# Optimization experiments

Hardware: AMD Instinct MI355X
Metric: run time of the kernel (lower is better)

## Reference

```python
import jax, jax.numpy as jnp
import numpy as np

TAU = 0.5

def setup_inputs() -> dict:
    key = jax.random.key(0)
    ks = jax.random.split(key, 8)
    B_Nq, B_Ns, C, H, W = 16, 16, 512, 32, 32
    f_q = jax.random.normal(ks[0], (B_Nq, C, H, W), dtype=jnp.float32)
    f_s = jax.random.normal(ks[1], (B_Ns, C, H, W), dtype=jnp.float32)
    # depthwise 1x1 convs with groups=dim, bias=False -> per-channel scalar weights [C]
    w_cca_q = jax.random.normal(ks[2], (C,), dtype=jnp.float32)
    w_cca_k = jax.random.normal(ks[3], (C,), dtype=jnp.float32)
    w_cca_v = jax.random.normal(ks[4], (C,), dtype=jnp.float32)
    w_sca_q = jax.random.normal(ks[5], (C,), dtype=jnp.float32)
    w_sca_k = jax.random.normal(ks[6], (C,), dtype=jnp.float32)
    lam = jnp.float32(0.1)
    return {"f_q": f_q, "f_s": f_s, "w_cca_q": w_cca_q, "w_cca_k": w_cca_k,
            "w_cca_v": w_cca_v, "w_sca_q": w_sca_q, "w_sca_k": w_sca_k, "lam": lam}

def _dw(x, w):
    # depthwise 1x1 conv, no bias == per-channel scale; x: [B,C,H,W], w: [C]
    return x * w[None, :, None, None]

def reference(f_q, f_s, w_cca_q, w_cca_k, w_cca_v, w_sca_q, w_sca_k, lam):
    B_Nq, C, H, W = f_q.shape
    B_Ns = f_s.shape[0]
    P = H * W
    qc = _dw(f_q, w_cca_q).reshape(B_Nq, C, P)          # [B,C,P]
    kc_mean = _dw(f_s, w_cca_k).reshape(B_Ns, C, P).mean(axis=0)  # [C,P]
    vc_mean = _dw(f_s, w_cca_v).reshape(B_Ns, C, P).mean(axis=0)  # [C,P]
    # channel attention: [B,C,C]
    Ac = jax.nn.softmax(jnp.einsum('bcp,dp->bcd', qc, kc_mean) / P, axis=-1)
    f_cca_q = jnp.einsum('bcd,dp->bcp', Ac, vc_mean).reshape(B_Nq, C, H, W)
    qs = _dw(f_cca_q, w_sca_q).reshape(B_Nq, C, P)      # [B,C,P]
    ks_mean = _dw(f_s, w_sca_k).reshape(B_Ns, C, P).mean(axis=0)  # [C,P]
    # spatial affinity: [B,P,P]
    M = jnp.einsum('bcp,cq->bpq', qs, ks_mean) / (TAU * C)
    alpha = jax.nn.softmax(M.mean(axis=-1), axis=-1)    # [B_Nq,P]
    beta = jax.nn.softmax(M.mean(axis=-2), axis=-1)     # [B_Nq,P]
    beta_mean = jnp.broadcast_to(beta.mean(axis=0, keepdims=True), (B_Ns, P))
    Fq_out = f_q + lam * f_cca_q
    return (Fq_out, alpha, beta_mean)
```

## Files before the change

### kernel.cpp

```cpp
#include <hip/hip_runtime.h>

typedef __bf16 bf16;
typedef __bf16 bf16x4 __attribute__((ext_vector_type(4)));
typedef __bf16 bf16x8 __attribute__((ext_vector_type(8)));
typedef float f32x4 __attribute__((ext_vector_type(4)));


#define GLL16(g, l)                                                             \
    __builtin_amdgcn_global_load_lds((const __attribute__((address_space(1))) void*)(g), \
                                     (__attribute__((address_space(3))) void*)(l), 16, 0, 0)

__device__ inline float wave_reduce_sum(float v) {
#pragma unroll
    for (int m = 32; m >= 1; m >>= 1) v += __shfl_xor(v, m, 64);
    return v;
}
__device__ inline float wave_reduce_max(float v) {
#pragma unroll
    for (int m = 32; m >= 1; m >>= 1) v = fmaxf(v, __shfl_xor(v, m, 64));
    return v;
}

__global__ void k_prep(const float* __restrict__ fs, const float* __restrict__ fq,
                       float* __restrict__ fsm32, bf16* __restrict__ fsm16,
                       bf16* __restrict__ fsmT, bf16* __restrict__ fq16) {
    __shared__ bf16 tile[32][33];
    int bx = blockIdx.x, by = blockIdx.y;
    int p0 = bx * 32, c0 = by * 32;
    int t = threadIdx.x, tx = t & 31, ty = t >> 5;
#pragma unroll
    for (int i = 0; i < 4; ++i) {
        size_t off = (size_t)(c0 + ty + 8 * i) * 1024 + p0 + tx;
        float s = 0.f;
#pragma unroll
        for (int b = 0; b < 16; ++b) s += fs[(size_t)b * 524288 + off];
        s *= (1.f / 16.f);
        fsm32[off] = s;
        bf16 h = (bf16)s;
        fsm16[off] = h;
        tile[ty + 8 * i][tx] = h;
    }
    __syncthreads();
#pragma unroll
    for (int i = 0; i < 4; ++i)
        fsmT[(size_t)(p0 + ty + 8 * i) * 512 + c0 + tx] = tile[tx][ty + 8 * i];
    int blk = by * 32 + bx;
    const float4* f4 = (const float4*)fq;
#pragma unroll
    for (int i = 0; i < 16; ++i) {
        int idx = blk * 4096 + i * 256 + t;
        float4 v = f4[idx];
        bf16x4 h4 = {(bf16)v.x, (bf16)v.y, (bf16)v.z, (bf16)v.w};
        *(bf16x4*)(fq16 + (size_t)idx * 4) = h4;
    }
}

__global__ void k_u(const float* __restrict__ fsm32, const float* __restrict__ wsq,
                    const float* __restrict__ wsk, float* __restrict__ u,
                    float* __restrict__ rm) {
    int c = blockIdx.x;
    int t = threadIdx.x;
    float s = 0.f;
#pragma unroll
    for (int j = 0; j < 4; ++j) s += fsm32[(size_t)c * 1024 + t + 256 * j];
    s = wave_reduce_sum(s);
    __shared__ float red[4];
    int w = t >> 6, lane = t & 63;
    if (lane == 0) red[w] = s;
    __syncthreads();
    if (t == 0) {
        float rmv = (red[0] + red[1] + red[2] + red[3]) * (1.f / 1024.f);
        rm[c] = rmv;
        u[c] = wsq[c] * wsk[c] * rmv * (1.f / 256.f);
    }
}

__global__ void k_gemm1(const bf16* __restrict__ A, const bf16* __restrict__ B,
                        float* __restrict__ G) {
    __shared__ alignas(16) bf16 As[64 * 32];
    __shared__ alignas(16) bf16 Bs[128 * 32];
    const int dt = blockIdx.x, ct = blockIdx.y, b = blockIdx.z;
    const int t = threadIdx.x, w = t >> 6, lane = t & 63;
    const int quad = lane >> 4, r15 = lane & 15;
    const int wr = w & 1, wc = w >> 1;
    const bf16* Abase = A + ((size_t)(b * 512 + ct * 64)) * 1024;
    const bf16* Bbase = B + ((size_t)(dt * 128)) * 1024;
    const int pr = t >> 2;
    const int gc = (t & 3) ^ ((pr >> 1) & 3);
    f32x4 acc[2][4] = {};
    for (int k0 = 0; k0 < 1024; k0 += 32) {
        GLL16(Abase + (size_t)pr * 1024 + k0 + gc * 8, As + t * 8);
        GLL16(Bbase + (size_t)pr * 1024 + k0 + gc * 8, Bs + t * 8);
        GLL16(Bbase + (size_t)(pr + 64) * 1024 + k0 + gc * 8, Bs + (t + 256) * 8);
        __syncthreads();
        bf16x8 af[2], bfr[4];
#pragma unroll
        for (int mi = 0; mi < 2; ++mi) {
            int R = wr * 32 + mi * 16 + r15;
            int sc = quad ^ ((R >> 1) & 3);
            af[mi] = *(const bf16x8*)(As + R * 32 + sc * 8);
        }
#pragma unroll
        for (int j = 0; j < 4; ++j) {
            int R = wc * 64 + j * 16 + r15;
            int sc = quad ^ ((R >> 1) & 3);
            bfr[j] = *(const bf16x8*)(Bs + R * 32 + sc * 8);
        }
#pragma unroll
        for (int mi = 0; mi < 2; ++mi)
#pragma unroll
            for (int j = 0; j < 4; ++j)
                acc[mi][j] = __builtin_amdgcn_mfma_f32_16x16x32_bf16(af[mi], bfr[j], acc[mi][j], 0, 0, 0);
        __syncthreads();
    }
#pragma unroll
    for (int mi = 0; mi < 2; ++mi) {
        float* g = G + ((size_t)(b * 512 + ct * 64 + wr * 32 + mi * 16 + quad * 4)) * 512 +
                   dt * 128 + wc * 64 + r15;
#pragma unroll
        for (int j = 0; j < 4; ++j)
#pragma unroll
            for (int ii = 0; ii < 4; ++ii)
                g[(size_t)ii * 512 + j * 16] = acc[mi][j][ii];
    }
}

__global__ void k_softmax_ac(const float* __restrict__ G, const float* __restrict__ wq,
                             const float* __restrict__ wk, const float* __restrict__ wv,
                             const float* __restrict__ rm, bf16* __restrict__ Acw,
                             float* __restrict__ r) {
    int row = blockIdx.x * 4 + (threadIdx.x >> 6);
    int lane = threadIdx.x & 63;
    int c = row & 511;
    const float* g = G + (size_t)row * 512;
    float sc = wq[c] * (1.f / 1024.f);
    float v[8];
    float mx = -3.4e38f;
#pragma unroll
    for (int j = 0; j < 8; ++j) {
        int d = lane + 64 * j;
        v[j] = g[d] * sc * wk[d];
        mx = fmaxf(mx, v[j]);
    }
    mx = wave_reduce_max(mx);
    float sum = 0.f;
#pragma unroll
    for (int j = 0; j < 8; ++j) {
        v[j] = __expf(v[j] - mx);
        sum += v[j];
    }
    sum = wave_reduce_sum(sum);
    float inv = 1.f / sum;
    bf16* o = Acw + (size_t)row * 512;
    float rsum = 0.f;
#pragma unroll
    for (int j = 0; j < 8; ++j) {
        int d = lane + 64 * j;
        float aw = v[j] * inv * wv[d];
        o[d] = (bf16)aw;
        rsum += aw * rm[d];
    }
    rsum = wave_reduce_sum(rsum);
    if (lane == 0) r[row] = rsum;
}

__global__ void k_t(const bf16* __restrict__ Acw, const float* __restrict__ u,
                    float* __restrict__ tbp) {
    int half = blockIdx.z, b = blockIdx.y;
    int d = blockIdx.x * 256 + threadIdx.x;
    const bf16* base = Acw + (size_t)b * 262144 + (size_t)half * 256 * 512 + d;
    const float* uu = u + half * 256;
    float s0 = 0.f, s1 = 0.f, s2 = 0.f, s3 = 0.f;
#pragma unroll 4
    for (int c = 0; c < 256; c += 4) {
        s0 += uu[c] * (float)base[(size_t)c * 512];
        s1 += uu[c + 1] * (float)base[(size_t)(c + 1) * 512];
        s2 += uu[c + 2] * (float)base[(size_t)(c + 2) * 512];
        s3 += uu[c + 3] * (float)base[(size_t)(c + 3) * 512];
    }
    tbp[(half * 16 + b) * 512 + d] = (s0 + s1) + (s2 + s3);
}

__global__ void k_gemm2(const bf16* __restrict__ A, const bf16* __restrict__ B,
                        const float* __restrict__ fq, const float* __restrict__ lamp,
                        float* __restrict__ out) {
    __shared__ alignas(16) bf16 As[64 * 32];
    __shared__ alignas(16) bf16 Bs[128 * 32];
    const int pt = blockIdx.x, ct = blockIdx.y, b = blockIdx.z;
    const int t = threadIdx.x, w = t >> 6, lane = t & 63;
    const int quad = lane >> 4, r15 = lane & 15;
    const int wr = w & 1, wc = w >> 1;
    const bf16* Abase = A + ((size_t)(b * 512 + ct * 64)) * 512;
    const bf16* Bbase = B + ((size_t)(pt * 128)) * 512;
    const int pr = t >> 2;
    const int gc = (t & 3) ^ ((pr >> 1) & 3);
    f32x4 acc[2][4] = {};
    for (int k0 = 0; k0 < 512; k0 += 32) {
        GLL16(Abase + (size_t)pr * 512 + k0 + gc * 8, As + t * 8);
        GLL16(Bbase + (size_t)pr * 512 + k0 + gc * 8, Bs + t * 8);
        GLL16(Bbase + (size_t)(pr + 64) * 512 + k0 + gc * 8, Bs + (t + 256) * 8);
        __syncthreads();
        bf16x8 af[2], bfr[4];
#pragma unroll
        for (int mi = 0; mi < 2; ++mi) {
            int R = wr * 32 + mi * 16 + r15;
            int sc = quad ^ ((R >> 1) & 3);
            af[mi] = *(const bf16x8*)(As + R * 32 + sc * 8);
        }
#pragma unroll
        for (int j = 0; j < 4; ++j) {
            int R = wc * 64 + j * 16 + r15;
            int sc = quad ^ ((R >> 1) & 3);
            bfr[j] = *(const bf16x8*)(Bs + R * 32 + sc * 8);
        }
#pragma unroll
        for (int mi = 0; mi < 2; ++mi)
#pragma unroll
            for (int j = 0; j < 4; ++j)
                acc[mi][j] = __builtin_amdgcn_mfma_f32_16x16x32_bf16(af[mi], bfr[j], acc[mi][j], 0, 0, 0);
        __syncthreads();
    }
    float lam = lamp[0];
#pragma unroll
    for (int mi = 0; mi < 2; ++mi) {
        size_t rowbase = (size_t)(b * 512 + ct * 64 + wr * 32 + mi * 16 + quad * 4);
#pragma unroll
        for (int j = 0; j < 4; ++j)
#pragma unroll
            for (int ii = 0; ii < 4; ++ii) {
                size_t idx = (rowbase + ii) * 1024 + pt * 128 + wc * 64 + j * 16 + r15;
                out[idx] = fq[idx] + lam * acc[mi][j][ii];
            }
    }
}

__global__ void k_logits(const float* __restrict__ tbp, const float* __restrict__ r,
                         const float* __restrict__ wsq, const float* __restrict__ wsk,
                         const float* __restrict__ fsm32, float* __restrict__ alog,
                         float* __restrict__ blog) {
    int z = blockIdx.y, pq = blockIdx.x * 256 + threadIdx.x;
    if (z < 16) {
        const float* t0 = tbp + z * 512;
        const float* t1 = tbp + (16 + z) * 512;
        float s0 = 0.f, s1 = 0.f, s2 = 0.f, s3 = 0.f;
#pragma unroll 2
        for (int d = 0; d < 512; d += 4) {
            s0 += (t0[d] + t1[d]) * fsm32[(size_t)d * 1024 + pq];
            s1 += (t0[d + 1] + t1[d + 1]) * fsm32[(size_t)(d + 1) * 1024 + pq];
            s2 += (t0[d + 2] + t1[d + 2]) * fsm32[(size_t)(d + 2) * 1024 + pq];
            s3 += (t0[d + 3] + t1[d + 3]) * fsm32[(size_t)(d + 3) * 1024 + pq];
        }
        alog[z * 1024 + pq] = (s0 + s1) + (s2 + s3);
    } else {
        int b = z - 16;
        const float* rb = r + b * 512;
        float s0 = 0.f, s1 = 0.f, s2 = 0.f, s3 = 0.f;
#pragma unroll 2
        for (int c = 0; c < 512; c += 4) {
            s0 += rb[c] * wsq[c] * wsk[c] * (1.f / 256.f) * fsm32[(size_t)c * 1024 + pq];
            s1 += rb[c + 1] * wsq[c + 1] * wsk[c + 1] * (1.f / 256.f) * fsm32[(size_t)(c + 1) * 1024 + pq];
            s2 += rb[c + 2] * wsq[c + 2] * wsk[c + 2] * (1.f / 256.f) * fsm32[(size_t)(c + 2) * 1024 + pq];
            s3 += rb[c + 3] * wsq[c + 3] * wsk[c + 3] * (1.f / 256.f) * fsm32[(size_t)(c + 3) * 1024 + pq];
        }
        blog[b * 1024 + pq] = (s0 + s1) + (s2 + s3);
    }
}

__global__ void k_softmax_rows(const float* __restrict__ alog, const float* __restrict__ blog,
                               float* __restrict__ alpha_out, float* __restrict__ beta) {
    int z = blockIdx.x;
    int t = threadIdx.x;
    int w = t >> 6, lane = t & 63;
    const float* src = (z < 16) ? (alog + (size_t)z * 1024) : (blog + (size_t)(z - 16) * 1024);
    float v[4];
    float mx = -3.4e38f;
#pragma unroll
    for (int j = 0; j < 4; ++j) {
        v[j] = src[t + 256 * j];
        mx = fmaxf(mx, v[j]);
    }
    __shared__ float red[4];
    float wm = wave_reduce_max(mx);
    if (lane == 0) red[w] = wm;
    __syncthreads();
    mx = fmaxf(fmaxf(red[0], red[1]), fmaxf(red[2], red[3]));
    float s = 0.f;
#pragma unroll
    for (int j = 0; j < 4; ++j) {
        v[j] = __expf(v[j] - mx);
        s += v[j];
    }
    __syncthreads();
    float ws_ = wave_reduce_sum(s);
    if (lane == 0) red[w] = ws_;
    __syncthreads();
    s = red[0] + red[1] + red[2] + red[3];
    float inv = 1.f / s;
    if (z < 16) {
#pragma unroll
        for (int j = 0; j < 4; ++j) alpha_out[(size_t)z * 1024 + t + 256 * j] = v[j] * inv;
    } else {
#pragma unroll
        for (int j = 0; j < 4; ++j) beta[(size_t)(z - 16) * 1024 + t + 256 * j] = v[j] * inv;
    }
}

__global__ void k_betamean(const float* __restrict__ beta, float* __restrict__ out) {
    int q = blockIdx.x * 256 + threadIdx.x;
    float s = 0.f;
#pragma unroll
    for (int b = 0; b < 16; ++b) s += beta[b * 1024 + q];
    float val = s * (1.f / 16.f);
#pragma unroll
    for (int si = 0; si < 16; ++si) out[(size_t)si * 1024 + q] = val;
}

extern "C" void kernel_launch(void* const* d_in, const int* in_sizes, int n_in,
                              void* d_out, int out_size, void* d_ws, size_t ws_size,
                              hipStream_t stream) {
    const float* f_q = (const float*)d_in[0];
    const float* f_s = (const float*)d_in[1];
    const float* w_cca_q = (const float*)d_in[2];
    const float* w_cca_k = (const float*)d_in[3];
    const float* w_cca_v = (const float*)d_in[4];
    const float* w_sca_q = (const float*)d_in[5];
    const float* w_sca_k = (const float*)d_in[6];
    const float* lamp = (const float*)d_in[7];

    char* ws = (char*)d_ws;
    float* fsm32 = (float*)(ws + 0);
    bf16* fsm16 = (bf16*)(ws + 2097152);
    bf16* fsmT = (bf16*)(ws + 3145728);
    float* G = (float*)(ws + 4194304);
    bf16* Acw = (bf16*)(ws + 20971520);
    bf16* fq16 = (bf16*)(ws + 29360128);
    float* rm = (float*)(ws + 46137344);
    float* u = (float*)(ws + 46139392);
    float* r = (float*)(ws + 46141440);
    float* tbp = (float*)(ws + 46174208);
    float* alog = (float*)(ws + 46239744);
    float* blog = (float*)(ws + 46305280);
    float* beta = (float*)(ws + 46370816);

    float* out_fq = (float*)d_out;
    float* out_alpha = out_fq + 8388608;
    float* out_bmean = out_fq + 8404992;

    k_prep<<<dim3(32, 16), 256, 0, stream>>>(f_s, f_q, fsm32, fsm16, fsmT, fq16);
    k_u<<<512, 256, 0, stream>>>(fsm32, w_sca_q, w_sca_k, u, rm);
    k_gemm1<<<dim3(4, 8, 16), 256, 0, stream>>>(fq16, fsm16, G);
    k_softmax_ac<<<2048, 256, 0, stream>>>(G, w_cca_q, w_cca_k, w_cca_v, rm, Acw, r);
    k_t<<<dim3(2, 16, 2), 256, 0, stream>>>(Acw, u, tbp);
    k_gemm2<<<dim3(8, 8, 16), 256, 0, stream>>>(Acw, fsmT, f_q, lamp, out_fq);
    k_logits<<<dim3(4, 32), 256, 0, stream>>>(tbp, r, w_sca_q, w_sca_k, fsm32, alog, blog);
    k_softmax_rows<<<32, 256, 0, stream>>>(alog, blog, out_alpha, beta);
    k_betamean<<<4, 256, 0, stream>>>(beta, out_bmean);
}
```

Before: 202.6 us.

## Double-buffer GEMMs, fuse alpha logits into gemm2 epilogue, split beta logits

Both MFMA GEMMs now use a 64-wide K tile with two LDS buffers and an XOR swizzle, so the next tile loads while the current one computes. The k_t and k_logits kernels are removed. Alpha logits are computed in the gemm2 epilogue by reducing the accumulators against u and adding them with atomics. Beta logits move to a new kernel split over channels that also accumulates with atomics; the atomic buffers are zeroed inside k_softmax_ac. The prep kernel reads f_s with float4 loads. The atomics make summation order nondeterministic, and the alpha path now goes through the bf16 fsmT copy instead of fp32 fsm32.

```diff
diff --git a/kernel.cpp b/kernel.cpp
--- a/kernel.cpp
+++ b/kernel.cpp
@@ -27,20 +27,25 @@
     __shared__ bf16 tile[32][33];
     int bx = blockIdx.x, by = blockIdx.y;
     int p0 = bx * 32, c0 = by * 32;
-    int t = threadIdx.x, tx = t & 31, ty = t >> 5;
-#pragma unroll
-    for (int i = 0; i < 4; ++i) {
-        size_t off = (size_t)(c0 + ty + 8 * i) * 1024 + p0 + tx;
-        float s = 0.f;
-#pragma unroll
-        for (int b = 0; b < 16; ++b) s += fs[(size_t)b * 524288 + off];
-        s *= (1.f / 16.f);
-        fsm32[off] = s;
-        bf16 h = (bf16)s;
-        fsm16[off] = h;
-        tile[ty + 8 * i][tx] = h;
-    }
-    __syncthreads();
+    int t = threadIdx.x;
+    int cy = t >> 3, px = (t & 7) * 4;
+    size_t off = (size_t)(c0 + cy) * 1024 + p0 + px;
+    float4 s = {0.f, 0.f, 0.f, 0.f};
+#pragma unroll
+    for (int b = 0; b < 16; ++b) {
+        float4 v = *(const float4*)(fs + (size_t)b * 524288 + off);
+        s.x += v.x; s.y += v.y; s.z += v.z; s.w += v.w;
+    }
+    s.x *= (1.f / 16.f); s.y *= (1.f / 16.f); s.z *= (1.f / 16.f); s.w *= (1.f / 16.f);
+    *(float4*)(fsm32 + off) = s;
+    bf16x4 h4 = {(bf16)s.x, (bf16)s.y, (bf16)s.z, (bf16)s.w};
+    *(bf16x4*)(fsm16 + off) = h4;
+    tile[cy][px] = h4[0];
+    tile[cy][px + 1] = h4[1];
+    tile[cy][px + 2] = h4[2];
+    tile[cy][px + 3] = h4[3];
+    __syncthreads();
+    int tx = t & 31, ty = t >> 5;
 #pragma unroll
     for (int i = 0; i < 4; ++i)
         fsmT[(size_t)(p0 + ty + 8 * i) * 512 + c0 + tx] = tile[tx][ty + 8 * i];
@@ -50,8 +55,8 @@
     for (int i = 0; i < 16; ++i) {
         int idx = blk * 4096 + i * 256 + t;
         float4 v = f4[idx];
-        bf16x4 h4 = {(bf16)v.x, (bf16)v.y, (bf16)v.z, (bf16)v.w};
-        *(bf16x4*)(fq16 + (size_t)idx * 4) = h4;
+        bf16x4 q4 = {(bf16)v.x, (bf16)v.y, (bf16)v.z, (bf16)v.w};
+        *(bf16x4*)(fq16 + (size_t)idx * 4) = q4;
     }
 }
 
@@ -77,41 +82,58 @@
 
 __global__ void k_gemm1(const bf16* __restrict__ A, const bf16* __restrict__ B,
                         float* __restrict__ G) {
-    __shared__ alignas(16) bf16 As[64 * 32];
-    __shared__ alignas(16) bf16 Bs[128 * 32];
+    __shared__ alignas(16) bf16 As[2][64 * 64];
+    __shared__ alignas(16) bf16 Bs[2][128 * 64];
     const int dt = blockIdx.x, ct = blockIdx.y, b = blockIdx.z;
     const int t = threadIdx.x, w = t >> 6, lane = t & 63;
     const int quad = lane >> 4, r15 = lane & 15;
     const int wr = w & 1, wc = w >> 1;
     const bf16* Abase = A + ((size_t)(b * 512 + ct * 64)) * 1024;
     const bf16* Bbase = B + ((size_t)(dt * 128)) * 1024;
-    const int pr = t >> 2;
-    const int gc = (t & 3) ^ ((pr >> 1) & 3);
+    const int srow = t >> 3, schunk = t & 7;
     f32x4 acc[2][4] = {};
-    for (int k0 = 0; k0 < 1024; k0 += 32) {
-        GLL16(Abase + (size_t)pr * 1024 + k0 + gc * 8, As + t * 8);
-        GLL16(Bbase + (size_t)pr * 1024 + k0 + gc * 8, Bs + t * 8);
-        GLL16(Bbase + (size_t)(pr + 64) * 1024 + k0 + gc * 8, Bs + (t + 256) * 8);
+    auto STAGE = [&](int buf, int k0) {
+#pragma unroll
+        for (int i = 0; i < 2; ++i) {
+            int row = i * 32 + srow;
+            int gchunk = schunk ^ (row & 7);
+            GLL16(Abase + (size_t)row * 1024 + k0 + gchunk * 8, &As[buf][i * 2048 + t * 8]);
+        }
+#pragma unroll
+        for (int i = 0; i < 4; ++i) {
+            int row = i * 32 + srow;
+            int gchunk = schunk ^ (row & 7);
+            GLL16(Bbase + (size_t)row * 1024 + k0 + gchunk * 8, &Bs[buf][i * 2048 + t * 8]);
+        }
+    };
+    STAGE(0, 0);
+    __syncthreads();
+    int cur = 0;
+    for (int step = 0; step < 16; ++step) {
+        if (step < 15) STAGE(cur ^ 1, (step + 1) * 64);
+#pragma unroll
+        for (int ks = 0; ks < 2; ++ks) {
+            bf16x8 af[2], bfr[4];
+#pragma unroll
+            for (int mi = 0; mi < 2; ++mi) {
+                int R = wr * 32 + mi * 16 + r15;
+                int c = ks * 4 + quad;
+                af[mi] = *(const bf16x8*)(&As[cur][R * 64 + ((c ^ (R & 7)) * 8)]);
+            }
+#pragma unroll
+            for (int j = 0; j < 4; ++j) {
+                int R = wc * 64 + j * 16 + r15;
+                int c = ks * 4 + quad;
+                bfr[j] = *(const bf16x8*)(&Bs[cur][R * 64 + ((c ^ (R & 7)) * 8)]);
+            }
+#pragma unroll
+            for (int mi = 0; mi < 2; ++mi)
+#pragma unroll
+                for (int j = 0; j < 4; ++j)
+                    acc[mi][j] = __builtin_amdgcn_mfma_f32_16x16x32_bf16(af[mi], bfr[j], acc[mi][j], 0, 0, 0);
+        }
         __syncthreads();
-        bf16x8 af[2], bfr[4];
-#pragma unroll
-        for (int mi = 0; mi < 2; ++mi) {
-            int R = wr * 32 + mi * 16 + r15;
-            int sc = quad ^ ((R >> 1) & 3);
-            af[mi] = *(const bf16x8*)(As + R * 32 + sc * 8);
-        }
-#pragma unroll
-        for (int j = 0; j < 4; ++j) {
-            int R = wc * 64 + j * 16 + r15;
-            int sc = quad ^ ((R >> 1) & 3);
-            bfr[j] = *(const bf16x8*)(Bs + R * 32 + sc * 8);
-        }
-#pragma unroll
-        for (int mi = 0; mi < 2; ++mi)
-#pragma unroll
-            for (int j = 0; j < 4; ++j)
-                acc[mi][j] = __builtin_amdgcn_mfma_f32_16x16x32_bf16(af[mi], bfr[j], acc[mi][j], 0, 0, 0);
-        __syncthreads();
+        cur ^= 1;
     }
 #pragma unroll
     for (int mi = 0; mi < 2; ++mi) {
@@ -128,7 +150,8 @@
 __global__ void k_softmax_ac(const float* __restrict__ G, const float* __restrict__ wq,
                              const float* __restrict__ wk, const float* __restrict__ wv,
                              const float* __restrict__ rm, bf16* __restrict__ Acw,
-                             float* __restrict__ r) {
+                             float* __restrict__ r, float* __restrict__ zbuf) {
+    if (blockIdx.x < 128) zbuf[blockIdx.x * 256 + threadIdx.x] = 0.f;
     int row = blockIdx.x * 4 + (threadIdx.x >> 6);
     int lane = threadIdx.x & 63;
     int c = row & 511;
@@ -164,61 +187,62 @@
     if (lane == 0) r[row] = rsum;
 }
 
-__global__ void k_t(const bf16* __restrict__ Acw, const float* __restrict__ u,
-                    float* __restrict__ tbp) {
-    int half = blockIdx.z, b = blockIdx.y;
-    int d = blockIdx.x * 256 + threadIdx.x;
-    const bf16* base = Acw + (size_t)b * 262144 + (size_t)half * 256 * 512 + d;
-    const float* uu = u + half * 256;
-    float s0 = 0.f, s1 = 0.f, s2 = 0.f, s3 = 0.f;
-#pragma unroll 4
-    for (int c = 0; c < 256; c += 4) {
-        s0 += uu[c] * (float)base[(size_t)c * 512];
-        s1 += uu[c + 1] * (float)base[(size_t)(c + 1) * 512];
-        s2 += uu[c + 2] * (float)base[(size_t)(c + 2) * 512];
-        s3 += uu[c + 3] * (float)base[(size_t)(c + 3) * 512];
-    }
-    tbp[(half * 16 + b) * 512 + d] = (s0 + s1) + (s2 + s3);
-}
-
 __global__ void k_gemm2(const bf16* __restrict__ A, const bf16* __restrict__ B,
                         const float* __restrict__ fq, const float* __restrict__ lamp,
-                        float* __restrict__ out) {
-    __shared__ alignas(16) bf16 As[64 * 32];
-    __shared__ alignas(16) bf16 Bs[128 * 32];
+                        const float* __restrict__ u, float* __restrict__ out,
+                        float* __restrict__ alog) {
+    __shared__ alignas(16) bf16 As[2][64 * 64];
+    __shared__ alignas(16) bf16 Bs[2][128 * 64];
     const int pt = blockIdx.x, ct = blockIdx.y, b = blockIdx.z;
     const int t = threadIdx.x, w = t >> 6, lane = t & 63;
     const int quad = lane >> 4, r15 = lane & 15;
     const int wr = w & 1, wc = w >> 1;
     const bf16* Abase = A + ((size_t)(b * 512 + ct * 64)) * 512;
     const bf16* Bbase = B + ((size_t)(pt * 128)) * 512;
-    const int pr = t >> 2;
-    const int gc = (t & 3) ^ ((pr >> 1) & 3);
+    const int srow = t >> 3, schunk = t & 7;
     f32x4 acc[2][4] = {};
-    for (int k0 = 0; k0 < 512; k0 += 32) {
-        GLL16(Abase + (size_t)pr * 512 + k0 + gc * 8, As + t * 8);
-        GLL16(Bbase + (size_t)pr * 512 + k0 + gc * 8, Bs + t * 8);
-        GLL16(Bbase + (size_t)(pr + 64) * 512 + k0 + gc * 8, Bs + (t + 256) * 8);
+    auto STAGE = [&](int buf, int k0) {
+#pragma unroll
+        for (int i = 0; i < 2; ++i) {
+            int row = i * 32 + srow;
+            int gchunk = schunk ^ (row & 7);
+            GLL16(Abase + (size_t)row * 512 + k0 + gchunk * 8, &As[buf][i * 2048 + t * 8]);
+        }
+#pragma unroll
+        for (int i = 0; i < 4; ++i) {
+            int row = i * 32 + srow;
+            int gchunk = schunk ^ (row & 7);
+            GLL16(Bbase + (size_t)row * 512 + k0 + gchunk * 8, &Bs[buf][i * 2048 + t * 8]);
+        }
+    };
+    STAGE(0, 0);
+    __syncthreads();
+    int cur = 0;
+    for (int step = 0; step < 8; ++step) {
+        if (step < 7) STAGE(cur ^ 1, (step + 1) * 64);
+#pragma unroll
+        for (int ks = 0; ks < 2; ++ks) {
+            bf16x8 af[2], bfr[4];
+#pragma unroll
+            for (int mi = 0; mi < 2; ++mi) {
+                int R = wr * 32 + mi * 16 + r15;
+                int c = ks * 4 + quad;
+                af[mi] = *(const bf16x8*)(&As[cur][R * 64 + ((c ^ (R & 7)) * 8)]);
+            }
+#pragma unroll
+            for (int j = 0; j < 4; ++j) {
+                int R = wc * 64 + j * 16 + r15;
+                int c = ks * 4 + quad;
+                bfr[j] = *(const bf16x8*)(&Bs[cur][R * 64 + ((c ^ (R & 7)) * 8)]);
+            }
+#pragma unroll
+            for (int mi = 0; mi < 2; ++mi)
+#pragma unroll
+                for (int j = 0; j < 4; ++j)
+                    acc[mi][j] = __builtin_amdgcn_mfma_f32_16x16x32_bf16(af[mi], bfr[j], acc[mi][j], 0, 0, 0);
+        }
         __syncthreads();
-        bf16x8 af[2], bfr[4];
-#pragma unroll
-        for (int mi = 0; mi < 2; ++mi) {
-            int R = wr * 32 + mi * 16 + r15;
-            int sc = quad ^ ((R >> 1) & 3);
-            af[mi] = *(const bf16x8*)(As + R * 32 + sc * 8);
-        }
-#pragma unroll
-        for (int j = 0; j < 4; ++j) {
-            int R = wc * 64 + j * 16 + r15;
-            int sc = quad ^ ((R >> 1) & 3);
-            bfr[j] = *(const bf16x8*)(Bs + R * 32 + sc * 8);
-        }
-#pragma unroll
-        for (int mi = 0; mi < 2; ++mi)
-#pragma unroll
-            for (int j = 0; j < 4; ++j)
-                acc[mi][j] = __builtin_amdgcn_mfma_f32_16x16x32_bf16(af[mi], bfr[j], acc[mi][j], 0, 0, 0);
-        __syncthreads();
+        cur ^= 1;
     }
     float lam = lamp[0];
 #pragma unroll
@@ -232,38 +256,43 @@
                 out[idx] = fq[idx] + lam * acc[mi][j][ii];
             }
     }
-}
-
-__global__ void k_logits(const float* __restrict__ tbp, const float* __restrict__ r,
-                         const float* __restrict__ wsq, const float* __restrict__ wsk,
-                         const float* __restrict__ fsm32, float* __restrict__ alog,
-                         float* __restrict__ blog) {
-    int z = blockIdx.y, pq = blockIdx.x * 256 + threadIdx.x;
-    if (z < 16) {
-        const float* t0 = tbp + z * 512;
-        const float* t1 = tbp + (16 + z) * 512;
-        float s0 = 0.f, s1 = 0.f, s2 = 0.f, s3 = 0.f;
-#pragma unroll 2
-        for (int d = 0; d < 512; d += 4) {
-            s0 += (t0[d] + t1[d]) * fsm32[(size_t)d * 1024 + pq];
-            s1 += (t0[d + 1] + t1[d + 1]) * fsm32[(size_t)(d + 1) * 1024 + pq];
-            s2 += (t0[d + 2] + t1[d + 2]) * fsm32[(size_t)(d + 2) * 1024 + pq];
-            s3 += (t0[d + 3] + t1[d + 3]) * fsm32[(size_t)(d + 3) * 1024 + pq];
-        }
-        alog[z * 1024 + pq] = (s0 + s1) + (s2 + s3);
-    } else {
-        int b = z - 16;
-        const float* rb = r + b * 512;
-        float s0 = 0.f, s1 = 0.f, s2 = 0.f, s3 = 0.f;
-#pragma unroll 2
-        for (int c = 0; c < 512; c += 4) {
-            s0 += rb[c] * wsq[c] * wsk[c] * (1.f / 256.f) * fsm32[(size_t)c * 1024 + pq];
-            s1 += rb[c + 1] * wsq[c + 1] * wsk[c + 1] * (1.f / 256.f) * fsm32[(size_t)(c + 1) * 1024 + pq];
-            s2 += rb[c + 2] * wsq[c + 2] * wsk[c + 2] * (1.f / 256.f) * fsm32[(size_t)(c + 2) * 1024 + pq];
-            s3 += rb[c + 3] * wsq[c + 3] * wsk[c + 3] * (1.f / 256.f) * fsm32[(size_t)(c + 3) * 1024 + pq];
-        }
-        blog[b * 1024 + pq] = (s0 + s1) + (s2 + s3);
-    }
+    float uv[2][4];
+#pragma unroll
+    for (int mi = 0; mi < 2; ++mi)
+#pragma unroll
+        for (int ii = 0; ii < 4; ++ii)
+            uv[mi][ii] = u[ct * 64 + wr * 32 + mi * 16 + quad * 4 + ii];
+#pragma unroll
+    for (int j = 0; j < 4; ++j) {
+        float pv = 0.f;
+#pragma unroll
+        for (int mi = 0; mi < 2; ++mi)
+#pragma unroll
+            for (int ii = 0; ii < 4; ++ii)
+                pv += uv[mi][ii] * acc[mi][j][ii];
+        pv += __shfl_xor(pv, 16, 64);
+        pv += __shfl_xor(pv, 32, 64);
+        if (lane < 16)
+            atomicAdd(alog + (size_t)b * 1024 + pt * 128 + wc * 64 + j * 16 + r15, pv);
+    }
+}
+
+__global__ void k_blog(const float* __restrict__ r, const float* __restrict__ wsq,
+                       const float* __restrict__ wsk, const float* __restrict__ fsm32,
+                       float* __restrict__ blog) {
+    int pq = blockIdx.x * 256 + threadIdx.x;
+    int b = blockIdx.y;
+    int c0 = blockIdx.z * 128;
+    const float* rb = r + b * 512;
+    float s0 = 0.f, s1 = 0.f, s2 = 0.f, s3 = 0.f;
+#pragma unroll 4
+    for (int c = c0; c < c0 + 128; c += 4) {
+        s0 += rb[c] * wsq[c] * wsk[c] * fsm32[(size_t)c * 1024 + pq];
+        s1 += rb[c + 1] * wsq[c + 1] * wsk[c + 1] * fsm32[(size_t)(c + 1) * 1024 + pq];
+        s2 += rb[c + 2] * wsq[c + 2] * wsk[c + 2] * fsm32[(size_t)(c + 2) * 1024 + pq];
+        s3 += rb[c + 3] * wsq[c + 3] * wsk[c + 3] * fsm32[(size_t)(c + 3) * 1024 + pq];
+    }
+    atomicAdd(&blog[(size_t)b * 1024 + pq], ((s0 + s1) + (s2 + s3)) * (1.f / 256.f));
 }
 
 __global__ void k_softmax_rows(const float* __restrict__ alog, const float* __restrict__ blog,
@@ -337,7 +366,6 @@
     float* rm = (float*)(ws + 46137344);
     float* u = (float*)(ws + 46139392);
     float* r = (float*)(ws + 46141440);
-    float* tbp = (float*)(ws + 46174208);
     float* alog = (float*)(ws + 46239744);
     float* blog = (float*)(ws + 46305280);
     float* beta = (float*)(ws + 46370816);
@@ -349,10 +377,9 @@
     k_prep<<<dim3(32, 16), 256, 0, stream>>>(f_s, f_q, fsm32, fsm16, fsmT, fq16);
     k_u<<<512, 256, 0, stream>>>(fsm32, w_sca_q, w_sca_k, u, rm);
     k_gemm1<<<dim3(4, 8, 16), 256, 0, stream>>>(fq16, fsm16, G);
-    k_softmax_ac<<<2048, 256, 0, stream>>>(G, w_cca_q, w_cca_k, w_cca_v, rm, Acw, r);
-    k_t<<<dim3(2, 16, 2), 256, 0, stream>>>(Acw, u, tbp);
-    k_gemm2<<<dim3(8, 8, 16), 256, 0, stream>>>(Acw, fsmT, f_q, lamp, out_fq);
-    k_logits<<<dim3(4, 32), 256, 0, stream>>>(tbp, r, w_sca_q, w_sca_k, fsm32, alog, blog);
+    k_softmax_ac<<<2048, 256, 0, stream>>>(G, w_cca_q, w_cca_k, w_cca_v, rm, Acw, r, alog);
+    k_gemm2<<<dim3(8, 8, 16), 256, 0, stream>>>(Acw, fsmT, f_q, lamp, u, out_fq, alog);
+    k_blog<<<dim3(4, 16, 4), 256, 0, stream>>>(r, w_sca_q, w_sca_k, fsm32, blog);
     k_softmax_rows<<<32, 256, 0, stream>>>(alog, blog, out_alpha, beta);
     k_betamean<<<4, 256, 0, stream>>>(beta, out_bmean);
 }
```

Result: faster. 181.8 us (-10.3%).
